# Performance work log

Measured on AMD Instinct MI355X. Metric: run time of the kernel, lower is better.

The kernel has to match this reference:

```python
import jax, jax.numpy as jnp
import numpy as np

INPUT, HIDDEN, OUTPUT, SEQ = 128, 128, 128, 2048
BATCH = 256

def setup_inputs() -> dict:
    key = jax.random.key(0)
    ks = jax.random.split(key, 6)
    s_x = 1.0 / np.sqrt(INPUT)
    s_h = 1.0 / np.sqrt(HIDDEN)
    return {
        "x": jax.random.normal(ks[0], (BATCH, SEQ, INPUT), jnp.float32),
        "h0": jnp.zeros((BATCH, HIDDEN), jnp.float32),
        # weights stored as [in, out] so forward is x @ W + b (same math as torch Linear)
        "W_xh": jax.random.uniform(ks[1], (INPUT, HIDDEN), jnp.float32, -s_x, s_x),
        "b_xh": jax.random.uniform(ks[2], (HIDDEN,), jnp.float32, -s_x, s_x),
        "W_hh": jax.random.uniform(ks[3], (HIDDEN, HIDDEN), jnp.float32, -s_h, s_h),
        "W_out": jax.random.uniform(ks[4], (HIDDEN, OUTPUT), jnp.float32, -s_h, s_h),
        "b_out": jax.random.uniform(ks[5], (OUTPUT,), jnp.float32, -s_h, s_h),
    }

def reference(x, h0, W_xh, b_xh, W_hh, W_out, b_out):
    # Precompute input projections for all timesteps in one big GEMM: [B,S,H]
    xh = jnp.einsum("bsi,ih->bsh", x, W_xh) + b_xh

    def step(h, xh_t):
        h = jnp.tanh(xh_t + h @ W_hh)
        return h, None

    # scan over time (strict sequential dependency)
    h_last, _ = jax.lax.scan(step, h0, jnp.swapaxes(xh, 0, 1))  # [S,B,H] scan
    # module returns only the last timestep's output projection
    return h_last @ W_out + b_out
```

## Files before the change

### kernel.cpp

```cpp
#include <hip/hip_runtime.h>
#include <hip/hip_bf16.h>


#define SEQ   2048
#define HID   128
#define BATCH 256
#define BD    16

typedef __attribute__((ext_vector_type(8))) short    short8;
typedef __attribute__((ext_vector_type(4))) float    f32x4;
typedef __attribute__((ext_vector_type(4))) float    f4;
typedef __attribute__((ext_vector_type(2))) unsigned u32x2;
typedef __attribute__((ext_vector_type(4))) unsigned u32x4;

union F8 { unsigned u[4]; short8 s; };

__device__ __forceinline__ unsigned pkbf(float a, float b) {
    union { __hip_bfloat16 h[2]; unsigned u; } t;
    t.h[0] = __float2bfloat16(a);
    t.h[1] = __float2bfloat16(b);
    return t.u;
}

__device__ __forceinline__ float blo(unsigned u) {
    union { unsigned v; float f; } t; t.v = u << 16; return t.f;
}
__device__ __forceinline__ float bhi(unsigned u) {
    union { unsigned v; float f; } t; t.v = u & 0xffff0000u; return t.f;
}

__device__ __forceinline__ float tanh_fast(float x) {
    float e = __builtin_amdgcn_exp2f(x * 2.8853900817779268f);
    return 1.0f - 2.0f * __builtin_amdgcn_rcpf(e + 1.0f);
}

__device__ __forceinline__ void block_sync() {
    asm volatile("s_waitcnt lgkmcnt(0)" ::: "memory");
    __builtin_amdgcn_s_barrier();
    asm volatile("" ::: "memory");
}

#define MFMA16(A,B,C) __builtin_amdgcn_mfma_f32_16x16x32_bf16((A),(B),(C),0,0,0)

__launch_bounds__(256, 1)
__global__ void xh_gemm_kernel(const float* __restrict__ x,
                               const float* __restrict__ Wxh,
                               const float* __restrict__ bxh,
                               __hip_bfloat16* __restrict__ xh)
{
    const int tid  = threadIdx.x;
    const int wv   = tid >> 6;
    const int lane = tid & 63;
    const int lg   = lane >> 4;
    const int lm   = lane & 15;

    const int gw = blockIdx.x * 4 + wv;
    const int NW = gridDim.x * 4;
    const int NT = (BATCH * SEQ) / 16;

    short8 wa[8][4];
    {
        #pragma unroll
        for (int T = 0; T < 8; ++T) {
            #pragma unroll
            for (int c = 0; c < 4; ++c) {
                F8 f;
                #pragma unroll
                for (int e2 = 0; e2 < 4; ++e2) {
                    int k = 32*c + 8*lg + 2*e2;
                    f.u[e2] = pkbf(Wxh[(size_t)k*HID + 16*T + lm],
                                   Wxh[(size_t)(k+1)*HID + 16*T + lm]);
                }
                wa[T][c] = f.s;
            }
        }
    }
    float bb[8][4];
    #pragma unroll
    for (int T = 0; T < 8; ++T)
        #pragma unroll
        for (int r = 0; r < 4; ++r)
            bb[T][r] = bxh[16*T + 4*lg + r];

    for (int tile = gw; tile < NT; tile += NW) {
        const float* xp = x + (size_t)tile*16*HID + (size_t)lm*HID + 8*lg;
        f4 s[8];
        #pragma unroll
        for (int c = 0; c < 4; ++c) {
            s[2*c]   = *(const f4*)(xp + 32*c);
            s[2*c+1] = *(const f4*)(xp + 32*c + 4);
        }
        F8 xf[4];
        #pragma unroll
        for (int c = 0; c < 4; ++c) {
            xf[c].u[0] = pkbf(s[2*c][0],   s[2*c][1]);
            xf[c].u[1] = pkbf(s[2*c][2],   s[2*c][3]);
            xf[c].u[2] = pkbf(s[2*c+1][0], s[2*c+1][1]);
            xf[c].u[3] = pkbf(s[2*c+1][2], s[2*c+1][3]);
        }
        __hip_bfloat16* op = xh + (size_t)(tile*16 + lm) * HID;
        #pragma unroll
        for (int T = 0; T < 8; ++T) {
            f32x4 acc = {bb[T][0], bb[T][1], bb[T][2], bb[T][3]};
            #pragma unroll
            for (int c = 0; c < 4; ++c)
                acc = MFMA16(wa[T][c], xf[c].s, acc);
            u32x2 w;
            w[0] = pkbf(acc[0], acc[1]);
            w[1] = pkbf(acc[2], acc[3]);
            *reinterpret_cast<u32x2*>(op + 16*T + 4*lg) = w;
        }
    }
}


#define REC_STEP(SLOT, P, POFF, TRT)                                          \
    {                                                                          \
        f32x4 a0, a1;                                                          \
        a0[0] = blo(SLOT[0]); a0[1] = bhi(SLOT[0]);                            \
        a0[2] = blo(SLOT[1]); a0[3] = bhi(SLOT[1]);                            \
        a1[0] = blo(SLOT[2]); a1[1] = bhi(SLOT[2]);                            \
        a1[2] = blo(SLOT[3]); a1[3] = bhi(SLOT[3]);                            \
        if ((TRT) + 4 < SEQ) SLOT = *(const u32x4*)(xq + (POFF)*256);          \
        block_sync();                         \
        const char* rb = lds + (P)*4096;                                       \
        short8 fA = *(const short8*)(rb + rdA);                                \
        short8 fB = *(const short8*)(rb + rdB);                                \
        short8 fC = *(const short8*)(rb + rdC);                                \
        f32x4 t0 = {0.f,0.f,0.f,0.f}, t1 = {0.f,0.f,0.f,0.f};                  \
               \
        a0 = MFMA16(whhf[0][3], selffrag, a0);                                 \
        a1 = MFMA16(whhf[1][3], selffrag, a1);                                 \
        t0 = MFMA16(whhf[0][0], fA, t0);                                       \
        t1 = MFMA16(whhf[1][0], fA, t1);                                       \
        a0 = MFMA16(whhf[0][1], fB, a0);                                       \
        a1 = MFMA16(whhf[1][1], fB, a1);                                       \
        t0 = MFMA16(whhf[0][2], fC, t0);                                       \
        t1 = MFMA16(whhf[1][2], fC, t1);                                       \
        a0 += t0; a1 += t1;                                                    \
        F8 nf;                                                                 \
        nf.u[0] = pkbf(tanh_fast(a0[0]), tanh_fast(a0[1]));                    \
        nf.u[1] = pkbf(tanh_fast(a0[2]), tanh_fast(a0[3]));                    \
        nf.u[2] = pkbf(tanh_fast(a1[0]), tanh_fast(a1[1]));                    \
        nf.u[3] = pkbf(tanh_fast(a1[2]), tanh_fast(a1[3]));                    \
        selffrag = nf.s;                                                       \
        *reinterpret_cast<short8*>(lds + ((P)^1)*4096 + wrO) = selffrag;       \
    }

__launch_bounds__(256, 1)
__global__ void rnn_rec_kernel(const __hip_bfloat16* __restrict__ xh,
                               const float* __restrict__ h0,
                               const float* __restrict__ Whh,
                               const float* __restrict__ Wout,
                               const float* __restrict__ bout,
                               float* __restrict__ out)
{
    __shared__ __align__(16) char lds[2 * 4096];

    const int tid  = threadIdx.x;
    const int wv   = tid >> 6;
    const int lane = tid & 63;
    const int lg   = lane >> 4;
    const int lm   = lane & 15;
    const int b0   = blockIdx.x * BD;

    const int cA = (wv + 1) & 3, cB = (wv + 2) & 3, cC = (wv + 3) & 3;
    short8 whhf[2][4];
    {
        const int scol = 32*wv + 8*(lm >> 2) + (lm & 3);
        const int cs[4] = {cA, cB, cC, wv};
        #pragma unroll
        for (int u = 0; u < 2; ++u) {
            #pragma unroll
            for (int ci = 0; ci < 4; ++ci) {
                const int c = cs[ci];
                F8 f;
                #pragma unroll
                for (int e2 = 0; e2 < 4; ++e2) {
                    int k = 32*c + 8*lg + 2*e2;
                    f.u[e2] = pkbf(Whh[(size_t)k*HID + scol + 4*u],
                                   Whh[(size_t)(k+1)*HID + scol + 4*u]);
                }
                whhf[u][ci] = f.s;
            }
        }
    }

    const int rdA = cA*1024 + lane*16;
    const int rdB = cB*1024 + lane*16;
    const int rdC = cC*1024 + lane*16;
    const int wrO = wv*1024 + lane*16;

    short8 selffrag;
    {
        const float* hp = h0 + (size_t)(b0 + lm) * HID + 32*wv + 8*lg;
        f4 v0 = *(const f4*)(hp);
        f4 v1 = *(const f4*)(hp + 4);
        F8 f;
        f.u[0] = pkbf(v0[0], v0[1]); f.u[1] = pkbf(v0[2], v0[3]);
        f.u[2] = pkbf(v1[0], v1[1]); f.u[3] = pkbf(v1[2], v1[3]);
        selffrag = f.s;
        *reinterpret_cast<short8*>(lds + wrO) = selffrag;
    }

    const char* xq = (const char*)xh + (size_t)(b0 + lm) * SEQ * 256
                   + 64*wv + 16*lg;

    u32x4 sA = *(const u32x4*)(xq + 0*256);
    u32x4 sB = *(const u32x4*)(xq + 1*256);
    u32x4 sC = *(const u32x4*)(xq + 2*256);
    u32x4 sD = *(const u32x4*)(xq + 3*256);

    for (int t = 0; t < SEQ; t += 4) {
        REC_STEP(sA, 0, 4, t);
        REC_STEP(sB, 1, 5, t + 1);
        REC_STEP(sC, 0, 6, t + 2);
        REC_STEP(sD, 1, 7, t + 3);
        xq += 4 * 256;
    }

    block_sync();
    {
        short8 wof[2][4];
        const int col = 32*wv + lm;
        #pragma unroll
        for (int T = 0; T < 2; ++T) {
            #pragma unroll
            for (int c = 0; c < 4; ++c) {
                F8 f;
                #pragma unroll
                for (int e2 = 0; e2 < 4; ++e2) {
                    int k = 32*c + 8*lg + 2*e2;
                    f.u[e2] = pkbf(Wout[(size_t)k*HID + col + 16*T],
                                   Wout[(size_t)(k+1)*HID + col + 16*T]);
                }
                wof[T][c] = f.s;
            }
        }
        f32x4 o0 = {bout[32*wv + 4*lg + 0], bout[32*wv + 4*lg + 1],
                    bout[32*wv + 4*lg + 2], bout[32*wv + 4*lg + 3]};
        f32x4 o1 = {bout[32*wv + 16 + 4*lg + 0], bout[32*wv + 16 + 4*lg + 1],
                    bout[32*wv + 16 + 4*lg + 2], bout[32*wv + 16 + 4*lg + 3]};
        #pragma unroll
        for (int c = 0; c < 4; ++c) {
            short8 hf = *reinterpret_cast<const short8*>(lds + c*1024 + lane*16);
            o0 = MFMA16(wof[0][c], hf, o0);
            o1 = MFMA16(wof[1][c], hf, o1);
        }
        float* op = out + (size_t)(b0 + lm) * HID + 32*wv + 4*lg;
        *reinterpret_cast<f4*>(op)      = o0;
        *reinterpret_cast<f4*>(op + 16) = o1;
    }
}

#define RNN_STEP(SLOT, P, POFF, TRT)                                          \
    {                                                                          \
        F8 xf[4];                                                              \
        _Pragma("unroll")                                                      \
        for (int c = 0; c < 4; ++c) {                                          \
            xf[c].u[0] = pkbf(SLOT[2*c][0],   SLOT[2*c][1]);                   \
            xf[c].u[1] = pkbf(SLOT[2*c][2],   SLOT[2*c][3]);                   \
            xf[c].u[2] = pkbf(SLOT[2*c+1][0], SLOT[2*c+1][1]);                 \
            xf[c].u[3] = pkbf(SLOT[2*c+1][2], SLOT[2*c+1][3]);                 \
        }                                                                      \
        if ((TRT) + 2 < SEQ) {                                                 \
            _Pragma("unroll")                                                  \
            for (int c = 0; c < 4; ++c) {                                      \
                SLOT[2*c]   = *(const f4*)(xq + (POFF)*HID + 32*c);            \
                SLOT[2*c+1] = *(const f4*)(xq + (POFF)*HID + 32*c + 4);        \
            }                                                                  \
        }                                                                      \
        f32x4 a0 = {bx[0][0], bx[0][1], bx[0][2], bx[0][3]};                   \
        f32x4 a1 = {bx[1][0], bx[1][1], bx[1][2], bx[1][3]};                   \
        _Pragma("unroll")                                                      \
        for (int c = 0; c < 4; ++c) {                                          \
            a0 = MFMA16(wxh[0][c], xf[c].s, a0);                               \
            a1 = MFMA16(wxh[1][c], xf[c].s, a1);                               \
        }                                                                      \
        block_sync();                                                          \
        _Pragma("unroll")                                                      \
        for (int c = 0; c < 4; ++c) {                                          \
            short8 hf = *reinterpret_cast<const short8*>(lds + (P)*4096 + rd[c]); \
            a0 = MFMA16(whh[0][c], hf, a0);                                    \
            a1 = MFMA16(whh[1][c], hf, a1);                                    \
        }                                                                      \
        u32x2 w0, w1;                                                          \
        w0[0] = pkbf(tanh_fast(a0[0]), tanh_fast(a0[1]));                      \
        w0[1] = pkbf(tanh_fast(a0[2]), tanh_fast(a0[3]));                      \
        w1[0] = pkbf(tanh_fast(a1[0]), tanh_fast(a1[1]));                      \
        w1[1] = pkbf(tanh_fast(a1[2]), tanh_fast(a1[3]));                      \
        *reinterpret_cast<u32x2*>(lds + ((P)^1)*4096 + hw[0]) = w0;            \
        *reinterpret_cast<u32x2*>(lds + ((P)^1)*4096 + hw[1]) = w1;            \
    }

__launch_bounds__(256, 1)
__global__ void rnn_fused_kernel(const float* __restrict__ x,
                                 const float* __restrict__ h0,
                                 const float* __restrict__ Wxh,
                                 const float* __restrict__ bxh,
                                 const float* __restrict__ Whh,
                                 const float* __restrict__ Wout,
                                 const float* __restrict__ bout,
                                 float* __restrict__ out)
{
    __shared__ __align__(16) char lds[2 * 4096];

    const int tid  = threadIdx.x;
    const int wv   = tid >> 6;
    const int lane = tid & 63;
    const int lg   = lane >> 4;
    const int lm   = lane & 15;
    const int b0   = blockIdx.x * BD;

    short8 wxh[2][4], whh[2][4];
    {
        const int col = 32*wv + lm;
        #pragma unroll
        for (int T = 0; T < 2; ++T) {
            #pragma unroll
            for (int c = 0; c < 4; ++c) {
                F8 fx, fh;
                #pragma unroll
                for (int e2 = 0; e2 < 4; ++e2) {
                    int k = 32*c + 8*lg + 2*e2;
                    fx.u[e2] = pkbf(Wxh[(size_t)k*HID + col + 16*T],
                                    Wxh[(size_t)(k+1)*HID + col + 16*T]);
                    fh.u[e2] = pkbf(Whh[(size_t)k*HID + col + 16*T],
                                    Whh[(size_t)(k+1)*HID + col + 16*T]);
                }
                wxh[T][c] = fx.s; whh[T][c] = fh.s;
            }
        }
    }
    float bx[2][4];
    #pragma unroll
    for (int T = 0; T < 2; ++T)
        #pragma unroll
        for (int r = 0; r < 4; ++r)
            bx[T][r] = bxh[32*wv + 16*T + 4*lg + r];

    int rd[4];
    #pragma unroll
    for (int c = 0; c < 4; ++c)
        rd[c] = (lm*256 + 64*c + 16*lg) ^ ((lm & 7) << 4);
    int hw[2];
    #pragma unroll
    for (int T = 0; T < 2; ++T)
        hw[T] = (lm*256 + 2*(32*wv + 16*T + 4*lg)) ^ ((lm & 7) << 4);

    {
        int b  = tid >> 4;
        int j0 = (tid & 15) * 8;
        const float* hp = h0 + (size_t)(b0 + b) * HID + j0;
        f4 v0 = *(const f4*)(hp);
        f4 v1 = *(const f4*)(hp + 4);
        F8 f;
        f.u[0] = pkbf(v0[0], v0[1]); f.u[1] = pkbf(v0[2], v0[3]);
        f.u[2] = pkbf(v1[0], v1[1]); f.u[3] = pkbf(v1[2], v1[3]);
        int off = (b*256 + 2*j0) ^ ((b & 7) << 4);
        *reinterpret_cast<short8*>(lds + off) = f.s;
    }

    const float* xq = x + (size_t)(b0 + lm) * SEQ * HID + 8*lg;
    f4 sA[8], sB[8];
    #pragma unroll
    for (int c = 0; c < 4; ++c) {
        sA[2*c]   = *(const f4*)(xq + 32*c);
        sA[2*c+1] = *(const f4*)(xq + 32*c + 4);
        sB[2*c]   = *(const f4*)(xq + HID + 32*c);
        sB[2*c+1] = *(const f4*)(xq + HID + 32*c + 4);
    }

    for (int t = 0; t < SEQ; t += 2) {
        RNN_STEP(sA, 0, 2, t);
        RNN_STEP(sB, 1, 3, t + 1);
        xq += 2 * HID;
    }

    block_sync();
    {
        short8 wo[2][4];
        const int col = 32*wv + lm;
        #pragma unroll
        for (int T = 0; T < 2; ++T) {
            #pragma unroll
            for (int c = 0; c < 4; ++c) {
                F8 f;
                #pragma unroll
                for (int e2 = 0; e2 < 4; ++e2) {
                    int k = 32*c + 8*lg + 2*e2;
                    f.u[e2] = pkbf(Wout[(size_t)k*HID + col + 16*T],
                                   Wout[(size_t)(k+1)*HID + col + 16*T]);
                }
                wo[T][c] = f.s;
            }
        }
        f32x4 o0 = {bout[32*wv + 4*lg + 0], bout[32*wv + 4*lg + 1],
                    bout[32*wv + 4*lg + 2], bout[32*wv + 4*lg + 3]};
        f32x4 o1 = {bout[32*wv + 16 + 4*lg + 0], bout[32*wv + 16 + 4*lg + 1],
                    bout[32*wv + 16 + 4*lg + 2], bout[32*wv + 16 + 4*lg + 3]};
        #pragma unroll
        for (int c = 0; c < 4; ++c) {
            short8 hf = *reinterpret_cast<const short8*>(lds + rd[c]);
            o0 = MFMA16(wo[0][c], hf, o0);
            o1 = MFMA16(wo[1][c], hf, o1);
        }
        float* op = out + (size_t)(b0 + lm) * HID + 32*wv + 4*lg;
        *reinterpret_cast<f4*>(op)      = o0;
        *reinterpret_cast<f4*>(op + 16) = o1;
    }
}

extern "C" void kernel_launch(void* const* d_in, const int* in_sizes, int n_in,
                              void* d_out, int out_size, void* d_ws, size_t ws_size,
                              hipStream_t stream) {
    const float* x    = (const float*)d_in[0];
    const float* h0   = (const float*)d_in[1];
    const float* Wxh  = (const float*)d_in[2];
    const float* bxh  = (const float*)d_in[3];
    const float* Whh  = (const float*)d_in[4];
    const float* Wout = (const float*)d_in[5];
    const float* bout = (const float*)d_in[6];
    (void)in_sizes; (void)n_in; (void)out_size;

    const size_t need = (size_t)BATCH * SEQ * HID * 2;
    if (ws_size >= need) {
        __hip_bfloat16* xh = (__hip_bfloat16*)d_ws;
        xh_gemm_kernel<<<dim3(512), dim3(256), 0, stream>>>(x, Wxh, bxh, xh);
        rnn_rec_kernel<<<dim3(BATCH / BD), dim3(256), 0, stream>>>(
            xh, h0, Whh, Wout, bout, (float*)d_out);
    } else {
        rnn_fused_kernel<<<dim3(BATCH / BD), dim3(256), 0, stream>>>(
            x, h0, Wxh, bxh, Whh, Wout, bout, (float*)d_out);
    }
}
```

Before: 1.057 ms.

## Process two batch tiles per block in recurrence to interleave independent chains

The recurrence kernel now handles 32 batch rows per block as two independent 16-row tiles, each with its own LDS double buffer, register state and xh prefetch slots. The two tiles' MFMAs are interleaved within each timestep so independent work fills MFMA and LDS latency, and one block barrier per step serves both tiles. This halves the grid to 8 blocks and doubles per-step work and register pressure per wave.

New measurement: 1.552 ms. 1.47x slower.

```diff
diff --git a/kernel.cpp b/kernel.cpp
--- a/kernel.cpp
+++ b/kernel.cpp
@@ -114,55 +114,82 @@
 }
 
 
-#define REC_STEP(SLOT, P, POFF, TRT)                                          \
+#define REC2T_STEP(SA, SB, P, POFF, TRT)                                      \
     {                                                                          \
-        f32x4 a0, a1;                                                          \
-        a0[0] = blo(SLOT[0]); a0[1] = bhi(SLOT[0]);                            \
-        a0[2] = blo(SLOT[1]); a0[3] = bhi(SLOT[1]);                            \
-        a1[0] = blo(SLOT[2]); a1[1] = bhi(SLOT[2]);                            \
-        a1[2] = blo(SLOT[3]); a1[3] = bhi(SLOT[3]);                            \
-        if ((TRT) + 4 < SEQ) SLOT = *(const u32x4*)(xq + (POFF)*256);          \
-        block_sync();                         \
-        const char* rb = lds + (P)*4096;                                       \
-        short8 fA = *(const short8*)(rb + rdA);                                \
-        short8 fB = *(const short8*)(rb + rdB);                                \
-        short8 fC = *(const short8*)(rb + rdC);                                \
-        f32x4 t0 = {0.f,0.f,0.f,0.f}, t1 = {0.f,0.f,0.f,0.f};                  \
-               \
-        a0 = MFMA16(whhf[0][3], selffrag, a0);                                 \
-        a1 = MFMA16(whhf[1][3], selffrag, a1);                                 \
-        t0 = MFMA16(whhf[0][0], fA, t0);                                       \
-        t1 = MFMA16(whhf[1][0], fA, t1);                                       \
-        a0 = MFMA16(whhf[0][1], fB, a0);                                       \
-        a1 = MFMA16(whhf[1][1], fB, a1);                                       \
-        t0 = MFMA16(whhf[0][2], fC, t0);                                       \
-        t1 = MFMA16(whhf[1][2], fC, t1);                                       \
-        a0 += t0; a1 += t1;                                                    \
-        F8 nf;                                                                 \
-        nf.u[0] = pkbf(tanh_fast(a0[0]), tanh_fast(a0[1]));                    \
-        nf.u[1] = pkbf(tanh_fast(a0[2]), tanh_fast(a0[3]));                    \
-        nf.u[2] = pkbf(tanh_fast(a1[0]), tanh_fast(a1[1]));                    \
-        nf.u[3] = pkbf(tanh_fast(a1[2]), tanh_fast(a1[3]));                    \
-        selffrag = nf.s;                                                       \
-        *reinterpret_cast<short8*>(lds + ((P)^1)*4096 + wrO) = selffrag;       \
+        f32x4 aA0, aA1, aB0, aB1;                                              \
+        aA0[0] = blo(SA[0]); aA0[1] = bhi(SA[0]);                              \
+        aA0[2] = blo(SA[1]); aA0[3] = bhi(SA[1]);                              \
+        aA1[0] = blo(SA[2]); aA1[1] = bhi(SA[2]);                              \
+        aA1[2] = blo(SA[3]); aA1[3] = bhi(SA[3]);                              \
+        aB0[0] = blo(SB[0]); aB0[1] = bhi(SB[0]);                              \
+        aB0[2] = blo(SB[1]); aB0[3] = bhi(SB[1]);                              \
+        aB1[0] = blo(SB[2]); aB1[1] = bhi(SB[2]);                              \
+        aB1[2] = blo(SB[3]); aB1[3] = bhi(SB[3]);                              \
+        if ((TRT) + 4 < SEQ) {                                                 \
+            SA = *(const u32x4*)(xqA + (POFF)*256);                            \
+            SB = *(const u32x4*)(xqB + (POFF)*256);                            \
+        }                                                                      \
+        block_sync();           \
+        {                                                                      \
+            const char* rbA = ldsA + (P)*4096;                                 \
+            const char* rbB = ldsB + (P)*4096;                                 \
+            short8 fA0 = *(const short8*)(rbA + rd0);                          \
+            short8 fB0 = *(const short8*)(rbB + rd0);                          \
+            short8 fA1 = *(const short8*)(rbA + rd1);                          \
+            short8 fB1 = *(const short8*)(rbB + rd1);                          \
+            short8 fA2 = *(const short8*)(rbA + rd2);                          \
+            short8 fB2 = *(const short8*)(rbB + rd2);                          \
+              \
+            aA0 = MFMA16(whhf[0][3], selfA, aA0);                              \
+            aA1 = MFMA16(whhf[1][3], selfA, aA1);                              \
+            aB0 = MFMA16(whhf[0][3], selfB, aB0);                              \
+            aB1 = MFMA16(whhf[1][3], selfB, aB1);                              \
+            aA0 = MFMA16(whhf[0][0], fA0, aA0);                                \
+            aA1 = MFMA16(whhf[1][0], fA0, aA1);                                \
+            aB0 = MFMA16(whhf[0][0], fB0, aB0);                                \
+            aB1 = MFMA16(whhf[1][0], fB0, aB1);                                \
+            aA0 = MFMA16(whhf[0][1], fA1, aA0);                                \
+            aA1 = MFMA16(whhf[1][1], fA1, aA1);                                \
+            aB0 = MFMA16(whhf[0][1], fB1, aB0);                                \
+            aB1 = MFMA16(whhf[1][1], fB1, aB1);                                \
+            aA0 = MFMA16(whhf[0][2], fA2, aA0);                                \
+            aA1 = MFMA16(whhf[1][2], fA2, aA1);                                \
+            aB0 = MFMA16(whhf[0][2], fB2, aB0);                                \
+            aB1 = MFMA16(whhf[1][2], fB2, aB1);                                \
+        }                                                                      \
+        F8 nA, nB;                                                             \
+        nA.u[0] = pkbf(tanh_fast(aA0[0]), tanh_fast(aA0[1]));                  \
+        nA.u[1] = pkbf(tanh_fast(aA0[2]), tanh_fast(aA0[3]));                  \
+        nA.u[2] = pkbf(tanh_fast(aA1[0]), tanh_fast(aA1[1]));                  \
+        nA.u[3] = pkbf(tanh_fast(aA1[2]), tanh_fast(aA1[3]));                  \
+        nB.u[0] = pkbf(tanh_fast(aB0[0]), tanh_fast(aB0[1]));                  \
+        nB.u[1] = pkbf(tanh_fast(aB0[2]), tanh_fast(aB0[3]));                  \
+        nB.u[2] = pkbf(tanh_fast(aB1[0]), tanh_fast(aB1[1]));                  \
+        nB.u[3] = pkbf(tanh_fast(aB1[2]), tanh_fast(aB1[3]));                  \
+        selfA = nA.s;                                                          \
+        selfB = nB.s;                                                          \
+        *reinterpret_cast<short8*>(ldsA + ((P)^1)*4096 + wrO) = selfA;         \
+        *reinterpret_cast<short8*>(ldsB + ((P)^1)*4096 + wrO) = selfB;         \
     }
 
 __launch_bounds__(256, 1)
-__global__ void rnn_rec_kernel(const __hip_bfloat16* __restrict__ xh,
-                               const float* __restrict__ h0,
-                               const float* __restrict__ Whh,
-                               const float* __restrict__ Wout,
-                               const float* __restrict__ bout,
-                               float* __restrict__ out)
+__global__ void rnn_rec2t_kernel(const __hip_bfloat16* __restrict__ xh,
+                                 const float* __restrict__ h0,
+                                 const float* __restrict__ Whh,
+                                 const float* __restrict__ Wout,
+                                 const float* __restrict__ bout,
+                                 float* __restrict__ out)
 {
-    __shared__ __align__(16) char lds[2 * 4096];
+    __shared__ __align__(16) char lds[4 * 4096];
+    char* ldsA = lds;
+    char* ldsB = lds + 2 * 4096;
 
     const int tid  = threadIdx.x;
     const int wv   = tid >> 6;
     const int lane = tid & 63;
     const int lg   = lane >> 4;
     const int lm   = lane & 15;
-    const int b0   = blockIdx.x * BD;
+    const int b0   = blockIdx.x * 32;
 
     const int cA = (wv + 1) & 3, cB = (wv + 2) & 3, cC = (wv + 3) & 3;
     short8 whhf[2][4];
@@ -186,37 +213,47 @@
         }
     }
 
-    const int rdA = cA*1024 + lane*16;
-    const int rdB = cB*1024 + lane*16;
-    const int rdC = cC*1024 + lane*16;
+    const int rd0 = cA*1024 + lane*16;
+    const int rd1 = cB*1024 + lane*16;
+    const int rd2 = cC*1024 + lane*16;
     const int wrO = wv*1024 + lane*16;
 
-    short8 selffrag;
-    {
-        const float* hp = h0 + (size_t)(b0 + lm) * HID + 32*wv + 8*lg;
-        f4 v0 = *(const f4*)(hp);
-        f4 v1 = *(const f4*)(hp + 4);
-        F8 f;
-        f.u[0] = pkbf(v0[0], v0[1]); f.u[1] = pkbf(v0[2], v0[3]);
-        f.u[2] = pkbf(v1[0], v1[1]); f.u[3] = pkbf(v1[2], v1[3]);
-        selffrag = f.s;
-        *reinterpret_cast<short8*>(lds + wrO) = selffrag;
-    }
-
-    const char* xq = (const char*)xh + (size_t)(b0 + lm) * SEQ * 256
-                   + 64*wv + 16*lg;
-
-    u32x4 sA = *(const u32x4*)(xq + 0*256);
-    u32x4 sB = *(const u32x4*)(xq + 1*256);
-    u32x4 sC = *(const u32x4*)(xq + 2*256);
-    u32x4 sD = *(const u32x4*)(xq + 3*256);
+    short8 selfA, selfB;
+    {
+        const float* hpA = h0 + (size_t)(b0 + lm) * HID + 32*wv + 8*lg;
+        const float* hpB = hpA + (size_t)16 * HID;
+        f4 a0 = *(const f4*)(hpA), a1 = *(const f4*)(hpA + 4);
+        f4 b0v = *(const f4*)(hpB), b1 = *(const f4*)(hpB + 4);
+        F8 fa, fb;
+        fa.u[0] = pkbf(a0[0], a0[1]);  fa.u[1] = pkbf(a0[2], a0[3]);
+        fa.u[2] = pkbf(a1[0], a1[1]);  fa.u[3] = pkbf(a1[2], a1[3]);
+        fb.u[0] = pkbf(b0v[0], b0v[1]); fb.u[1] = pkbf(b0v[2], b0v[3]);
+        fb.u[2] = pkbf(b1[0], b1[1]);  fb.u[3] = pkbf(b1[2], b1[3]);
+        selfA = fa.s; selfB = fb.s;
+        *reinterpret_cast<short8*>(ldsA + wrO) = selfA;
+        *reinterpret_cast<short8*>(ldsB + wrO) = selfB;
+    }
+
+    const char* xqA = (const char*)xh + (size_t)(b0 + lm) * SEQ * 256
+                    + 64*wv + 16*lg;
+    const char* xqB = xqA + (size_t)16 * SEQ * 256;
+
+    u32x4 sA0 = *(const u32x4*)(xqA + 0*256);
+    u32x4 sA1 = *(const u32x4*)(xqA + 1*256);
+    u32x4 sA2 = *(const u32x4*)(xqA + 2*256);
+    u32x4 sA3 = *(const u32x4*)(xqA + 3*256);
+    u32x4 sB0 = *(const u32x4*)(xqB + 0*256);
+    u32x4 sB1 = *(const u32x4*)(xqB + 1*256);
+    u32x4 sB2 = *(const u32x4*)(xqB + 2*256);
+    u32x4 sB3 = *(const u32x4*)(xqB + 3*256);
 
     for (int t = 0; t < SEQ; t += 4) {
-        REC_STEP(sA, 0, 4, t);
-        REC_STEP(sB, 1, 5, t + 1);
-        REC_STEP(sC, 0, 6, t + 2);
-        REC_STEP(sD, 1, 7, t + 3);
-        xq += 4 * 256;
+        REC2T_STEP(sA0, sB0, 0, 4, t);
+        REC2T_STEP(sA1, sB1, 1, 5, t + 1);
+        REC2T_STEP(sA2, sB2, 0, 6, t + 2);
+        REC2T_STEP(sA3, sB3, 1, 7, t + 3);
+        xqA += 4 * 256;
+        xqB += 4 * 256;
     }
 
     block_sync();
@@ -237,19 +274,23 @@
                 wof[T][c] = f.s;
             }
         }
-        f32x4 o0 = {bout[32*wv + 4*lg + 0], bout[32*wv + 4*lg + 1],
-                    bout[32*wv + 4*lg + 2], bout[32*wv + 4*lg + 3]};
-        f32x4 o1 = {bout[32*wv + 16 + 4*lg + 0], bout[32*wv + 16 + 4*lg + 1],
-                    bout[32*wv + 16 + 4*lg + 2], bout[32*wv + 16 + 4*lg + 3]};
-        #pragma unroll
-        for (int c = 0; c < 4; ++c) {
-            short8 hf = *reinterpret_cast<const short8*>(lds + c*1024 + lane*16);
-            o0 = MFMA16(wof[0][c], hf, o0);
-            o1 = MFMA16(wof[1][c], hf, o1);
-        }
-        float* op = out + (size_t)(b0 + lm) * HID + 32*wv + 4*lg;
-        *reinterpret_cast<f4*>(op)      = o0;
-        *reinterpret_cast<f4*>(op + 16) = o1;
+        #pragma unroll
+        for (int tl = 0; tl < 2; ++tl) {
+            const char* hb = (tl == 0) ? ldsA : ldsB;
+            f32x4 o0 = {bout[32*wv + 4*lg + 0], bout[32*wv + 4*lg + 1],
+                        bout[32*wv + 4*lg + 2], bout[32*wv + 4*lg + 3]};
+            f32x4 o1 = {bout[32*wv + 16 + 4*lg + 0], bout[32*wv + 16 + 4*lg + 1],
+                        bout[32*wv + 16 + 4*lg + 2], bout[32*wv + 16 + 4*lg + 3]};
+            #pragma unroll
+            for (int c = 0; c < 4; ++c) {
+                short8 hf = *reinterpret_cast<const short8*>(hb + c*1024 + lane*16);
+                o0 = MFMA16(wof[0][c], hf, o0);
+                o1 = MFMA16(wof[1][c], hf, o1);
+            }
+            float* op = out + (size_t)(b0 + 16*tl + lm) * HID + 32*wv + 4*lg;
+            *reinterpret_cast<f4*>(op)      = o0;
+            *reinterpret_cast<f4*>(op + 16) = o1;
+        }
     }
 }
 
@@ -427,7 +468,7 @@
     if (ws_size >= need) {
         __hip_bfloat16* xh = (__hip_bfloat16*)d_ws;
         xh_gemm_kernel<<<dim3(512), dim3(256), 0, stream>>>(x, Wxh, bxh, xh);
-        rnn_rec_kernel<<<dim3(BATCH / BD), dim3(256), 0, stream>>>(
+        rnn_rec2t_kernel<<<dim3(BATCH / 32), dim3(256), 0, stream>>>(
             xh, h0, Whh, Wout, bout, (float*)d_out);
     } else {
         rnn_fused_kernel<<<dim3(BATCH / BD), dim3(256), 0, stream>>>(
```

## Switch recurrence to split-K partial-sum exchange through LDS

Applied to the files above, without the earlier changes.

Each wave now holds a K-slice of W_hh matching its own hidden chunk and computes partial products for all output columns from its own h fragment. It writes the fp32 partials for other waves to LDS, synchronizes once, then sums the received partials before tanh. The goal is to start MFMAs before the barrier so MFMA work overlaps the sync latency instead of waiting on the neighbours' h. In exchange it moves more LDS traffic per step (fp32 partials instead of bf16 h) and needs a larger double-buffered LDS area.

Measured after the change: 1.046 ms. Within noise of the previous version (-1.0%).

```diff
diff --git a/kernel.cpp b/kernel.cpp
--- a/kernel.cpp
+++ b/kernel.cpp
@@ -114,48 +114,63 @@
 }
 
 
-#define REC_STEP(SLOT, P, POFF, TRT)                                          \
+#define RECSK_STEP(S, P, POFF, TRT)                                           \
     {                                                                          \
-        f32x4 a0, a1;                                                          \
-        a0[0] = blo(SLOT[0]); a0[1] = bhi(SLOT[0]);                            \
-        a0[2] = blo(SLOT[1]); a0[3] = bhi(SLOT[1]);                            \
-        a1[0] = blo(SLOT[2]); a1[1] = bhi(SLOT[2]);                            \
-        a1[2] = blo(SLOT[3]); a1[3] = bhi(SLOT[3]);                            \
-        if ((TRT) + 4 < SEQ) SLOT = *(const u32x4*)(xq + (POFF)*256);          \
-        block_sync();                         \
-        const char* rb = lds + (P)*4096;                                       \
-        short8 fA = *(const short8*)(rb + rdA);                                \
-        short8 fB = *(const short8*)(rb + rdB);                                \
-        short8 fC = *(const short8*)(rb + rdC);                                \
-        f32x4 t0 = {0.f,0.f,0.f,0.f}, t1 = {0.f,0.f,0.f,0.f};                  \
-               \
-        a0 = MFMA16(whhf[0][3], selffrag, a0);                                 \
-        a1 = MFMA16(whhf[1][3], selffrag, a1);                                 \
-        t0 = MFMA16(whhf[0][0], fA, t0);                                       \
-        t1 = MFMA16(whhf[1][0], fA, t1);                                       \
-        a0 = MFMA16(whhf[0][1], fB, a0);                                       \
-        a1 = MFMA16(whhf[1][1], fB, a1);                                       \
-        t0 = MFMA16(whhf[0][2], fC, t0);                                       \
-        t1 = MFMA16(whhf[1][2], fC, t1);                                       \
-        a0 += t0; a1 += t1;                                                    \
+        f32x4 own0, own1;                                                      \
+        own0[0] = blo(S[0]); own0[1] = bhi(S[0]);                              \
+        own0[2] = blo(S[1]); own0[3] = bhi(S[1]);                              \
+        own1[0] = blo(S[2]); own1[1] = bhi(S[2]);                              \
+        own1[2] = blo(S[3]); own1[3] = bhi(S[3]);                              \
+        if ((TRT) + 4 < SEQ) S = *(const u32x4*)(xq + (POFF)*256);             \
+        const f32x4 z = {0.f, 0.f, 0.f, 0.f};                                  \
+        f32x4 g0 = z, g1 = z, g2 = z, g3 = z, g4 = z, g5 = z;                  \
+                \
+        g0 = MFMA16(whfF[0], self, g0);                                        \
+        g1 = MFMA16(whfF[1], self, g1);                                        \
+        g2 = MFMA16(whfF[2], self, g2);                                        \
+        g3 = MFMA16(whfF[3], self, g3);                                        \
+        g4 = MFMA16(whfF[4], self, g4);                                        \
+        g5 = MFMA16(whfF[5], self, g5);                                        \
+        own0 = MFMA16(whfO[0], self, own0);                                    \
+        own1 = MFMA16(whfO[1], self, own1);                                    \
+        {                                                                      \
+            char* wb = lds + (P)*24576;                                        \
+            *reinterpret_cast<f32x4*>(wb + wz[0]) = g0;                        \
+            *reinterpret_cast<f32x4*>(wb + wz[1]) = g1;                        \
+            *reinterpret_cast<f32x4*>(wb + wz[2]) = g2;                        \
+            *reinterpret_cast<f32x4*>(wb + wz[3]) = g3;                        \
+            *reinterpret_cast<f32x4*>(wb + wz[4]) = g4;                        \
+            *reinterpret_cast<f32x4*>(wb + wz[5]) = g5;                        \
+        }                                                                      \
+        block_sync();                                                          \
+        {                                                                      \
+            const char* rb = lds + (P)*24576;                                  \
+            f32x4 p00 = *(const f32x4*)(rb + rz[0]);                           \
+            f32x4 p01 = *(const f32x4*)(rb + rz[1]);                           \
+            f32x4 p02 = *(const f32x4*)(rb + rz[2]);                           \
+            f32x4 p10 = *(const f32x4*)(rb + rz[3]);                           \
+            f32x4 p11 = *(const f32x4*)(rb + rz[4]);                           \
+            f32x4 p12 = *(const f32x4*)(rb + rz[5]);                           \
+            own0 += (p00 + p01) + p02;                                         \
+            own1 += (p10 + p11) + p12;                                         \
+        }                                                                      \
         F8 nf;                                                                 \
-        nf.u[0] = pkbf(tanh_fast(a0[0]), tanh_fast(a0[1]));                    \
-        nf.u[1] = pkbf(tanh_fast(a0[2]), tanh_fast(a0[3]));                    \
-        nf.u[2] = pkbf(tanh_fast(a1[0]), tanh_fast(a1[1]));                    \
-        nf.u[3] = pkbf(tanh_fast(a1[2]), tanh_fast(a1[3]));                    \
-        selffrag = nf.s;                                                       \
-        *reinterpret_cast<short8*>(lds + ((P)^1)*4096 + wrO) = selffrag;       \
+        nf.u[0] = pkbf(tanh_fast(own0[0]), tanh_fast(own0[1]));                \
+        nf.u[1] = pkbf(tanh_fast(own0[2]), tanh_fast(own0[3]));                \
+        nf.u[2] = pkbf(tanh_fast(own1[0]), tanh_fast(own1[1]));                \
+        nf.u[3] = pkbf(tanh_fast(own1[2]), tanh_fast(own1[3]));                \
+        self = nf.s;                                                           \
     }
 
 __launch_bounds__(256, 1)
-__global__ void rnn_rec_kernel(const __hip_bfloat16* __restrict__ xh,
-                               const float* __restrict__ h0,
-                               const float* __restrict__ Whh,
-                               const float* __restrict__ Wout,
-                               const float* __restrict__ bout,
-                               float* __restrict__ out)
+__global__ void rnn_recsk_kernel(const __hip_bfloat16* __restrict__ xh,
+                                 const float* __restrict__ h0,
+                                 const float* __restrict__ Whh,
+                                 const float* __restrict__ Wout,
+                                 const float* __restrict__ bout,
+                                 float* __restrict__ out)
 {
-    __shared__ __align__(16) char lds[2 * 4096];
+    __shared__ __align__(16) char lds[2 * 24576];
 
     const int tid  = threadIdx.x;
     const int wv   = tid >> 6;
@@ -164,34 +179,43 @@
     const int lm   = lane & 15;
     const int b0   = blockIdx.x * BD;
 
-    const int cA = (wv + 1) & 3, cB = (wv + 2) & 3, cC = (wv + 3) & 3;
-    short8 whhf[2][4];
-    {
-        const int scol = 32*wv + 8*(lm >> 2) + (lm & 3);
-        const int cs[4] = {cA, cB, cC, wv};
-        #pragma unroll
-        for (int u = 0; u < 2; ++u) {
-            #pragma unroll
-            for (int ci = 0; ci < 4; ++ci) {
-                const int c = cs[ci];
+    short8 whfO[2], whfF[6];
+    {
+        #pragma unroll
+        for (int i = 0; i < 4; ++i) {
+            const int w = (wv + i) & 3;
+            #pragma unroll
+            for (int u = 0; u < 2; ++u) {
+                const int scol = 32*w + 8*(lm >> 2) + 4*u + (lm & 3);
                 F8 f;
                 #pragma unroll
                 for (int e2 = 0; e2 < 4; ++e2) {
-                    int k = 32*c + 8*lg + 2*e2;
-                    f.u[e2] = pkbf(Whh[(size_t)k*HID + scol + 4*u],
-                                   Whh[(size_t)(k+1)*HID + scol + 4*u]);
+                    int k = 32*wv + 8*lg + 2*e2;
+                    f.u[e2] = pkbf(Whh[(size_t)k*HID + scol],
+                                   Whh[(size_t)(k+1)*HID + scol]);
                 }
-                whhf[u][ci] = f.s;
+                if (i == 0) whfO[u] = f.s;
+                else        whfF[2*(i-1) + u] = f.s;
             }
         }
     }
 
-    const int rdA = cA*1024 + lane*16;
-    const int rdB = cB*1024 + lane*16;
-    const int rdC = cC*1024 + lane*16;
-    const int wrO = wv*1024 + lane*16;
-
-    short8 selffrag;
+    int wz[6], rz[6];
+    #pragma unroll
+    for (int i = 0; i < 3; ++i) {
+        const int w   = (wv + 1 + i) & 3;
+        const int src = (wv - w - 1) & 3;
+        #pragma unroll
+        for (int u = 0; u < 2; ++u)
+            wz[2*i + u] = w*6144 + u*3072 + src*1024 + lane*16;
+    }
+    #pragma unroll
+    for (int u = 0; u < 2; ++u)
+        #pragma unroll
+        for (int s = 0; s < 3; ++s)
+            rz[3*u + s] = wv*6144 + u*3072 + s*1024 + lane*16;
+
+    short8 self;
     {
         const float* hp = h0 + (size_t)(b0 + lm) * HID + 32*wv + 8*lg;
         f4 v0 = *(const f4*)(hp);
@@ -199,8 +223,7 @@
         F8 f;
         f.u[0] = pkbf(v0[0], v0[1]); f.u[1] = pkbf(v0[2], v0[3]);
         f.u[2] = pkbf(v1[0], v1[1]); f.u[3] = pkbf(v1[2], v1[3]);
-        selffrag = f.s;
-        *reinterpret_cast<short8*>(lds + wrO) = selffrag;
+        self = f.s;
     }
 
     const char* xq = (const char*)xh + (size_t)(b0 + lm) * SEQ * 256
@@ -212,44 +235,43 @@
     u32x4 sD = *(const u32x4*)(xq + 3*256);
 
     for (int t = 0; t < SEQ; t += 4) {
-        REC_STEP(sA, 0, 4, t);
-        REC_STEP(sB, 1, 5, t + 1);
-        REC_STEP(sC, 0, 6, t + 2);
-        REC_STEP(sD, 1, 7, t + 3);
+        RECSK_STEP(sA, 0, 4, t);
+        RECSK_STEP(sB, 1, 5, t + 1);
+        RECSK_STEP(sC, 0, 6, t + 2);
+        RECSK_STEP(sD, 1, 7, t + 3);
         xq += 4 * 256;
     }
 
     block_sync();
-    {
-        short8 wof[2][4];
-        const int col = 32*wv + lm;
-        #pragma unroll
-        for (int T = 0; T < 2; ++T) {
+    *reinterpret_cast<short8*>(lds + wv*1024 + lane*16) = self;
+    block_sync();
+    {
+        short8 hf[4];
+        #pragma unroll
+        for (int c = 0; c < 4; ++c)
+            hf[c] = *reinterpret_cast<const short8*>(lds + c*1024 + lane*16);
+
+        #pragma unroll
+        for (int Tl = 0; Tl < 2; ++Tl) {
+            const int col = 32*wv + 16*Tl + lm;
+            f32x4 o = {bout[32*wv + 16*Tl + 4*lg + 0],
+                       bout[32*wv + 16*Tl + 4*lg + 1],
+                       bout[32*wv + 16*Tl + 4*lg + 2],
+                       bout[32*wv + 16*Tl + 4*lg + 3]};
             #pragma unroll
             for (int c = 0; c < 4; ++c) {
                 F8 f;
                 #pragma unroll
                 for (int e2 = 0; e2 < 4; ++e2) {
                     int k = 32*c + 8*lg + 2*e2;
-                    f.u[e2] = pkbf(Wout[(size_t)k*HID + col + 16*T],
-                                   Wout[(size_t)(k+1)*HID + col + 16*T]);
+                    f.u[e2] = pkbf(Wout[(size_t)k*HID + col],
+                                   Wout[(size_t)(k+1)*HID + col]);
                 }
-                wof[T][c] = f.s;
+                o = MFMA16(f.s, hf[c], o);
             }
-        }
-        f32x4 o0 = {bout[32*wv + 4*lg + 0], bout[32*wv + 4*lg + 1],
-                    bout[32*wv + 4*lg + 2], bout[32*wv + 4*lg + 3]};
-        f32x4 o1 = {bout[32*wv + 16 + 4*lg + 0], bout[32*wv + 16 + 4*lg + 1],
-                    bout[32*wv + 16 + 4*lg + 2], bout[32*wv + 16 + 4*lg + 3]};
-        #pragma unroll
-        for (int c = 0; c < 4; ++c) {
-            short8 hf = *reinterpret_cast<const short8*>(lds + c*1024 + lane*16);
-            o0 = MFMA16(wof[0][c], hf, o0);
-            o1 = MFMA16(wof[1][c], hf, o1);
-        }
-        float* op = out + (size_t)(b0 + lm) * HID + 32*wv + 4*lg;
-        *reinterpret_cast<f4*>(op)      = o0;
-        *reinterpret_cast<f4*>(op + 16) = o1;
+            float* op = out + (size_t)(b0 + lm) * HID + 32*wv + 16*Tl + 4*lg;
+            *reinterpret_cast<f4*>(op) = o;
+        }
     }
 }
 
@@ -427,7 +449,7 @@
     if (ws_size >= need) {
         __hip_bfloat16* xh = (__hip_bfloat16*)d_ws;
         xh_gemm_kernel<<<dim3(512), dim3(256), 0, stream>>>(x, Wxh, bxh, xh);
-        rnn_rec_kernel<<<dim3(BATCH / BD), dim3(256), 0, stream>>>(
+        rnn_recsk_kernel<<<dim3(BATCH / BD), dim3(256), 0, stream>>>(
             xh, h0, Whh, Wout, bout, (float*)d_out);
     } else {
         rnn_fused_kernel<<<dim3(BATCH / BD), dim3(256), 0, stream>>>(
```

## Replace per-step block barrier with LDS flag-based wave-to-wave synchronization

Applied to the files above, without the earlier changes.

The recurrence loop no longer calls a workgroup barrier at every timestep. Instead, each wave publishes a step counter in LDS after writing its hidden-state fragment, and spins until the three peer waves' counters reach the current step. The MFMA on the wave's own fragment is moved ahead of the wait so it overlaps the spin. This targets barrier latency on the strictly sequential critical path. The cost is busy-wait LDS polling, and correctness now depends on the double-buffer ordering together with explicit lgkmcnt waits.

New measurement: 1.899 ms. 79.6% more time.

```diff
diff --git a/kernel.cpp b/kernel.cpp
--- a/kernel.cpp
+++ b/kernel.cpp
@@ -114,23 +114,27 @@
 }
 
 
-#define REC_STEP(SLOT, P, POFF, TRT)                                          \
+#define RECFF_STEP(S, P, POFF, TRT)                                           \
     {                                                                          \
         f32x4 a0, a1;                                                          \
-        a0[0] = blo(SLOT[0]); a0[1] = bhi(SLOT[0]);                            \
-        a0[2] = blo(SLOT[1]); a0[3] = bhi(SLOT[1]);                            \
-        a1[0] = blo(SLOT[2]); a1[1] = bhi(SLOT[2]);                            \
-        a1[2] = blo(SLOT[3]); a1[3] = bhi(SLOT[3]);                            \
-        if ((TRT) + 4 < SEQ) SLOT = *(const u32x4*)(xq + (POFF)*256);          \
-        block_sync();                         \
+        a0[0] = blo(S[0]); a0[1] = bhi(S[0]);                                  \
+        a0[2] = blo(S[1]); a0[3] = bhi(S[1]);                                  \
+        a1[0] = blo(S[2]); a1[1] = bhi(S[2]);                                  \
+        a1[2] = blo(S[3]); a1[3] = bhi(S[3]);                                  \
+        if ((TRT) + 4 < SEQ) S = *(const u32x4*)(xq + (POFF)*256);             \
+              \
+        a0 = MFMA16(whhf[0][3], self, a0);                                     \
+        a1 = MFMA16(whhf[1][3], self, a1);                                     \
+        {                                                                      \
+            const int tgt = (TRT) + 1;                                         \
+            while (pfA[0] < tgt || pfB[0] < tgt || pfC[0] < tgt) { }           \
+        }                                                                      \
+        asm volatile("" ::: "memory");                                         \
         const char* rb = lds + (P)*4096;                                       \
         short8 fA = *(const short8*)(rb + rdA);                                \
         short8 fB = *(const short8*)(rb + rdB);                                \
         short8 fC = *(const short8*)(rb + rdC);                                \
         f32x4 t0 = {0.f,0.f,0.f,0.f}, t1 = {0.f,0.f,0.f,0.f};                  \
-               \
-        a0 = MFMA16(whhf[0][3], selffrag, a0);                                 \
-        a1 = MFMA16(whhf[1][3], selffrag, a1);                                 \
         t0 = MFMA16(whhf[0][0], fA, t0);                                       \
         t1 = MFMA16(whhf[1][0], fA, t1);                                       \
         a0 = MFMA16(whhf[0][1], fB, a0);                                       \
@@ -143,19 +147,21 @@
         nf.u[1] = pkbf(tanh_fast(a0[2]), tanh_fast(a0[3]));                    \
         nf.u[2] = pkbf(tanh_fast(a1[0]), tanh_fast(a1[1]));                    \
         nf.u[3] = pkbf(tanh_fast(a1[2]), tanh_fast(a1[3]));                    \
-        selffrag = nf.s;                                                       \
-        *reinterpret_cast<short8*>(lds + ((P)^1)*4096 + wrO) = selffrag;       \
+        self = nf.s;                                                           \
+        *reinterpret_cast<short8*>(lds + ((P)^1)*4096 + wrO) = self;           \
+        asm volatile("s_waitcnt lgkmcnt(0)" ::: "memory");                     \
+        if (lane == 0) myf[0] = (TRT) + 2;                                     \
     }
 
 __launch_bounds__(256, 1)
-__global__ void rnn_rec_kernel(const __hip_bfloat16* __restrict__ xh,
-                               const float* __restrict__ h0,
-                               const float* __restrict__ Whh,
-                               const float* __restrict__ Wout,
-                               const float* __restrict__ bout,
-                               float* __restrict__ out)
+__global__ void rnn_recff_kernel(const __hip_bfloat16* __restrict__ xh,
+                                 const float* __restrict__ h0,
+                                 const float* __restrict__ Whh,
+                                 const float* __restrict__ Wout,
+                                 const float* __restrict__ bout,
+                                 float* __restrict__ out)
 {
-    __shared__ __align__(16) char lds[2 * 4096];
+    __shared__ __align__(16) char lds[8192 + 16];
 
     const int tid  = threadIdx.x;
     const int wv   = tid >> 6;
@@ -191,7 +197,13 @@
     const int rdC = cC*1024 + lane*16;
     const int wrO = wv*1024 + lane*16;
 
-    short8 selffrag;
+    volatile int* flg = (volatile int*)(lds + 8192);
+    volatile int* myf = flg + wv;
+    volatile const int* pfA = flg + cA;
+    volatile const int* pfB = flg + cB;
+    volatile const int* pfC = flg + cC;
+
+    short8 self;
     {
         const float* hp = h0 + (size_t)(b0 + lm) * HID + 32*wv + 8*lg;
         f4 v0 = *(const f4*)(hp);
@@ -199,9 +211,12 @@
         F8 f;
         f.u[0] = pkbf(v0[0], v0[1]); f.u[1] = pkbf(v0[2], v0[3]);
         f.u[2] = pkbf(v1[0], v1[1]); f.u[3] = pkbf(v1[2], v1[3]);
-        selffrag = f.s;
-        *reinterpret_cast<short8*>(lds + wrO) = selffrag;
-    }
+        self = f.s;
+        *reinterpret_cast<short8*>(lds + wrO) = self;
+        asm volatile("s_waitcnt lgkmcnt(0)" ::: "memory");
+        if (lane == 0) myf[0] = 1;
+    }
+    block_sync();
 
     const char* xq = (const char*)xh + (size_t)(b0 + lm) * SEQ * 256
                    + 64*wv + 16*lg;
@@ -212,14 +227,18 @@
     u32x4 sD = *(const u32x4*)(xq + 3*256);
 
     for (int t = 0; t < SEQ; t += 4) {
-        REC_STEP(sA, 0, 4, t);
-        REC_STEP(sB, 1, 5, t + 1);
-        REC_STEP(sC, 0, 6, t + 2);
-        REC_STEP(sD, 1, 7, t + 3);
+        RECFF_STEP(sA, 0, 4, t);
+        RECFF_STEP(sB, 1, 5, t + 1);
+        RECFF_STEP(sC, 0, 6, t + 2);
+        RECFF_STEP(sD, 1, 7, t + 3);
         xq += 4 * 256;
     }
 
-    block_sync();
+    {
+        const int tgt = SEQ + 1;
+        while (pfA[0] < tgt || pfB[0] < tgt || pfC[0] < tgt) { }
+    }
+    asm volatile("" ::: "memory");
     {
         short8 wof[2][4];
         const int col = 32*wv + lm;
@@ -427,7 +446,7 @@
     if (ws_size >= need) {
         __hip_bfloat16* xh = (__hip_bfloat16*)d_ws;
         xh_gemm_kernel<<<dim3(512), dim3(256), 0, stream>>>(x, Wxh, bxh, xh);
-        rnn_rec_kernel<<<dim3(BATCH / BD), dim3(256), 0, stream>>>(
+        rnn_recff_kernel<<<dim3(BATCH / BD), dim3(256), 0, stream>>>(
             xh, h0, Whh, Wout, bout, (float*)d_out);
     } else {
         rnn_fused_kernel<<<dim3(BATCH / BD), dim3(256), 0, stream>>>(
```
